# Performance work log

Measured on AMD Instinct MI355X. Metric: run time of the kernel, lower is better.

The kernel has to match this reference:

```python
import jax, jax.numpy as jnp
import numpy as np
import math

B_GRAPHS = 256
L_NODES = 64
N_NODES = B_GRAPHS * L_NODES
N_EDGES = N_NODES * 4
HEADS = 8
D_INNER = 512
N_DAGS = 1
DIAMETER = 64


def setup_inputs() -> dict:
    key = jax.random.key(0)
    ks = jax.random.split(key, 8)
    x = jax.random.normal(ks[0], (N_NODES, D_INNER), jnp.float32)
    B = jax.random.normal(ks[1], (N_NODES, D_INNER), jnp.float32)
    C = jax.random.normal(ks[2], (N_NODES, D_INNER), jnp.float32)
    dt = jax.random.normal(ks[3], (N_NODES, N_DAGS * HEADS * 2), jnp.float32)
    dt_edge = jax.random.normal(ks[4], (N_EDGES, N_DAGS * HEADS), jnp.float32)
    # DAG edges: within each graph, src_local < dst_local (gap 1..7) -> strictly upper triangular
    u = jax.random.randint(ks[5], (N_EDGES,), 0, L_NODES - 1)
    gap = jax.random.randint(ks[6], (N_EDGES,), 1, 8)
    v = jnp.minimum(u + gap, L_NODES - 1)
    graph = jnp.arange(N_EDGES) // (N_EDGES // B_GRAPHS)
    edge_index = jnp.stack([graph * L_NODES + u, graph * L_NODES + v]).astype(jnp.int32)
    data_batch = (jnp.arange(N_NODES) // L_NODES).astype(jnp.int32)
    dag_masks = jnp.ones((N_DAGS, N_EDGES), jnp.float32)
    # dt_bias init as in module __init__ (inverse softplus of dt in [1e-3, 1e-1])
    rng = np.random.default_rng(0)
    dtv = np.exp(rng.uniform(size=(HEADS,)) * (math.log(0.1) - math.log(0.001)) + math.log(0.001))
    dtv = np.clip(dtv, 1e-4, None)
    dt_bias = jnp.asarray(dtv + np.log(-np.expm1(-dtv)), jnp.float32)
    D = jnp.ones((HEADS,), jnp.float32)
    return dict(x=x, B=B, C=C, dt=dt, dt_edge=dt_edge, dt_bias=dt_bias, D=D,
                dag_masks=dag_masks, edge_index=edge_index, data_batch=data_batch,
                diameter=DIAMETER)


def _repeated_squaring_inverse(A, diam):
    # (I - A)^{-1} = prod_k (I + A^{2^k}) for nilpotent A; O(log diam) matmuls
    j = 2 ** int(math.ceil(math.log2(diam)))
    I = jnp.eye(A.shape[-1], dtype=A.dtype)
    last = A
    M = I + A
    for _ in range(2, int(math.log2(j)) + 1):
        last = last @ last
        M = M @ (I + last)
    return M


def reference(x, B, C, dt, dt_edge, dt_bias, D, dag_masks, edge_index, data_batch, diameter):
    N, din = x.shape
    g, E = dag_masks.shape
    n = dt_bias.shape[0]
    b = int(data_batch[-1]) + 1
    l = N // b  # equal-size graphs -> dense batching is a reshape, mask all-True
    h = din // n
    src, dst = edge_index[0], edge_index[1]

    # dt_node: (N, g*n*c) -> (c, g, n, N); softplus(dt + bias)
    c = dt.shape[1] // (g * n)
    dtn = dt.reshape(N, g, n, c).transpose(3, 1, 2, 0)
    dtn = jax.nn.softplus(dtn + dt_bias[None, None, :, None])
    dte = dt_edge.reshape(E, g, n).transpose(1, 2, 0)  # (g,n,E)
    dte = jax.nn.softplus(dte + dt_bias[None, :, None])

    dt_s, dt_t = dtn[0], dtn[1]
    dt_sum = (dt_s[:, :, src] + dt_t[:, :, dst] + dte) / np.sqrt(3.0)  # (g,n,E)
    dt_exp = jnp.exp(-dt_sum)
    msk = dag_masks[:, None, :]
    dt_sum = dt_sum * msk
    dt_exp = dt_exp * msk

    # dense adjacency with per-edge attrs; note 'b l1 l2 (g n) -> b g n l2 l1' transpose
    b_e = src // l
    sl = src % l
    dl = dst % l
    attr = dt_exp.transpose(2, 0, 1).reshape(E, g * n)
    adj = jnp.zeros((b, l, l, g * n), x.dtype).at[b_e, sl, dl].add(attr)
    A = adj.reshape(b, l, l, g, n).transpose(0, 3, 4, 2, 1)  # (b,g,n,l,l)

    # normalize_mat: sqrt outer product of in-degree counts, clamped at 1
    ec = jnp.zeros((g, N), x.dtype).at[:, dst].add(dag_masks)
    ec_dense = ec.T.reshape(b, l, g)
    outer = jnp.sqrt(jnp.einsum('blg,btg->bglt', ec_dense, ec_dense))
    outer = jnp.where(outer < 1.0, 1.0, outer)
    A = A / outer[:, :, None]

    dnorm = jnp.zeros((g, n, N), x.dtype).at[:, :, dst].add(dt_sum)
    dnorm = dnorm.transpose(2, 0, 1).reshape(b, l, g, n).transpose(0, 2, 3, 1)  # (b,g,n,l)

    A2 = A.reshape(b, g * n, l, l).astype(jnp.float32)
    L = _repeated_squaring_inverse(A2, int(diameter))
    L = L.reshape(b, g, n, l, l) * dnorm[..., None]

    x4 = x.reshape(b, l, n, h).transpose(0, 2, 1, 3)  # (b,n,l,h)
    B3 = B.reshape(b, l, -1)
    C3 = C.reshape(b, l, -1)
    # y = einsum(C,L,B,x) with B/C broadcast over (g,n): fold C.B^T into L
    CB = jnp.einsum('bld,btd->blt', C3, B3)
    M = L * CB[:, None, None]
    y = jnp.einsum('bgnlt,bnth->bgnlh', M, x4)
    y = y + x4[:, None] * D[None, None, :, None, None]
    y = y.transpose(0, 3, 1, 2, 4).reshape(N, g, n * h)  # b g n l h -> (N, g, n*h)
    y = y.sum(axis=1) / np.sqrt(g)
    return y
```

## Files before the change

kernel.cpp:

```cpp
#include <hip/hip_runtime.h>
#include <math.h>

#define NGRAPH 256
#define LNODE  64
#define HEADS  8
#define DIN    512
#define EPG    256
#define NEDGE  65536

typedef short bf16x8 __attribute__((ext_vector_type(8)));
typedef float f32x4 __attribute__((ext_vector_type(4)));

__device__ __forceinline__ float softplusf(float v) {
    return (v > 20.f) ? v : log1pf(expf(v));
}
__device__ __forceinline__ unsigned short f2bf(float f) {
    union { float f; unsigned u; } c; c.f = f;
    unsigned r = c.u + 0x7fffu + ((c.u >> 16) & 1u);
    return (unsigned short)(r >> 16);
}
__device__ __forceinline__ float bf2f(unsigned short h) {
    union { float f; unsigned u; } c; c.u = ((unsigned)h) << 16;
    return c.f;
}

__global__ __launch_bounds__(256) void cb_kernel(const float* __restrict__ Bm,
                                                 const float* __restrict__ Cm,
                                                 float* __restrict__ CBp,
                                                 int dper, int tposed) {
    int b = blockIdx.x;
    int slice = blockIdx.y;
    __shared__ float Cs[64 * 68];
    __shared__ float Bs[64 * 68];
    int tid = threadIdx.x;
    int ti = tid >> 4, tj = tid & 15;
    float acc[4][4] = {};
    const float* Cg = Cm + (size_t)b * 64 * DIN;
    const float* Bg = Bm + (size_t)b * 64 * DIN;
    int d_lo = slice * dper;
    for (int d0 = d_lo; d0 < d_lo + dper; d0 += 64) {
        __syncthreads();
        #pragma unroll
        for (int k = 0; k < 4; ++k) {
            int f = k * 256 + tid;
            int row = f >> 4;
            int c4 = (f & 15) << 2;
            *(float4*)(Cs + row * 68 + c4) = *(const float4*)(Cg + row * DIN + d0 + c4);
            *(float4*)(Bs + row * 68 + c4) = *(const float4*)(Bg + row * DIN + d0 + c4);
        }
        __syncthreads();
        for (int d = 0; d < 64; d += 4) {
            float4 cr[4], br[4];
            #pragma unroll
            for (int r = 0; r < 4; ++r) cr[r] = *(const float4*)(Cs + (4 * ti + r) * 68 + d);
            #pragma unroll
            for (int c = 0; c < 4; ++c) br[c] = *(const float4*)(Bs + (4 * tj + c) * 68 + d);
            #pragma unroll
            for (int r = 0; r < 4; ++r)
                #pragma unroll
                for (int c = 0; c < 4; ++c)
                    acc[r][c] += cr[r].x * br[c].x + cr[r].y * br[c].y +
                                 cr[r].z * br[c].z + cr[r].w * br[c].w;
        }
    }
    float* outp = CBp + ((size_t)slice * NGRAPH + b) * 4096;
    if (!tposed) {
        #pragma unroll
        for (int r = 0; r < 4; ++r)
            *(float4*)(outp + (4 * ti + r) * 64 + 4 * tj) =
                make_float4(acc[r][0], acc[r][1], acc[r][2], acc[r][3]);
    } else {
        #pragma unroll
        for (int r = 0; r < 4; ++r)
            #pragma unroll
            for (int c = 0; c < 4; ++c)
                outp[(4 * tj + c) * 64 + (4 * ti + r)] = acc[r][c];
    }
}

__global__ __launch_bounds__(256, 5) void fused2_kernel(const float* __restrict__ x,
                                                        const float* __restrict__ dt,
                                                        const float* __restrict__ dt_edge,
                                                        const float* __restrict__ dt_bias,
                                                        const float* __restrict__ Dp,
                                                        const float* __restrict__ dag_masks,
                                                        const int* __restrict__ edge_index,
                                                        const float* __restrict__ CBp,
                                                        float* __restrict__ out,
                                                        int nslice) {
    int b = blockIdx.x;
    int head = blockIdx.y;
    __shared__ unsigned short CBsh[64 * 64];
    __shared__ unsigned short Wl[64 * 72];
    __shared__ unsigned short Xt[64 * 66];
    __shared__ float Ab[512];
    __shared__ float dnsh[64];
    __shared__ float ecsh[64];
    __shared__ float dts[64];
    __shared__ float dtt[64];
    int tid = threadIdx.x;
    int w = tid >> 6;
    int lane = tid & 63;
    float bias = dt_bias[head];
    const float* xg0 = x + (size_t)b * 64 * DIN + head * 64;

    if (w == 0) {
        for (int it = 0; it < 16; ++it) {
            int s4 = it * 64 + lane;
            float4 v = *(const float4*)(CBp + (size_t)b * 4096 + s4 * 4);
            for (int s = 1; s < nslice; ++s) {
                float4 p = *(const float4*)(CBp + ((size_t)s * NGRAPH + b) * 4096 + s4 * 4);
                v.x += p.x; v.y += p.y; v.z += p.z; v.w += p.w;
            }
            unsigned short* q = &CBsh[s4 * 4];
            q[0] = f2bf(v.x); q[1] = f2bf(v.y); q[2] = f2bf(v.z); q[3] = f2bf(v.w);
        }
    } else {
        for (int t = w - 1; t < 64; t += 3) {
            float v = xg0[(size_t)t * DIN + lane];
            Xt[lane * 66 + t] = f2bf(v);
        }
        if (w == 1) {
            int node = b * 64 + lane;
            dts[lane] = softplusf(dt[node * 16 + head * 2 + 0] + bias);
            dtt[lane] = softplusf(dt[node * 16 + head * 2 + 1] + bias);
        } else if (w == 2) {
            #pragma unroll
            for (int k = 0; k < 8; ++k) Ab[k * 64 + lane] = 0.f;
        } else {
            dnsh[lane] = 0.f;
            ecsh[lane] = 0.f;
        }
    }
    __syncthreads();

    {
        int e = b * EPG + tid;
        int sl = edge_index[e] & 63;
        int dl = edge_index[NEDGE + e] & 63;
        float mk = dag_masks[e];
        float de = softplusf(dt_edge[e * HEADS + head] + bias);
        float dsum = (dts[sl] + dtt[dl] + de) * 0.57735026918962576451f;
        float dexp = expf(-dsum);
        atomicAdd(&Ab[dl * 8 + (dl - sl)], dexp * mk);
        atomicAdd(&dnsh[dl], dsum * mk);
        atomicAdd(&ecsh[dl], mk);
    }
    __syncthreads();

    for (int k = tid; k < 512; k += 256) {
        int i = k >> 3, d = k & 7;
        int src = i - d;
        if (d >= 1 && src >= 0) {
            float den = sqrtf(ecsh[i] * ecsh[src]);
            if (den < 1.f) den = 1.f;
            Ab[k] = Ab[k] / den;
        }
    }
    __syncthreads();

    int m = lane & 15;
    int quad = lane >> 4;
    union { bf16x8 v; unsigned u[4]; } bf[4][2];
    #pragma unroll
    for (int eb = 0; eb < 4; ++eb) {
        int n66 = (eb * 16 + m) * 66;
        #pragma unroll
        for (int h = 0; h < 2; ++h) {
            int base = n66 + h * 32 + quad * 8;
            #pragma unroll
            for (int c = 0; c < 4; ++c)
                bf[eb][h].u[c] = *(const unsigned*)(&Xt[base + 2 * c]);
        }
    }
    if (w == 0) {
        int j = lane;
        float Dh = Dp[head];
        float mwin[7] = {0.f, 0.f, 0.f, 0.f, 0.f, 0.f, 0.f};
        for (int i = 0; i < 64; ++i) {
            float mi = (j == i) ? 1.f : 0.f;
            #pragma unroll
            for (int s = 0; s < 7; ++s) mi += Ab[i * 8 + s + 1] * mwin[s];
            float wv = mi * bf2f(CBsh[i * 64 + j]) * dnsh[i];
            if (j == i) wv += Dh;
            Wl[i * 72 + j] = f2bf(wv);
            #pragma unroll
            for (int s = 6; s > 0; --s) mwin[s] = mwin[s - 1];
            mwin[0] = mi;
        }
    }
    __syncthreads();

    {
        bf16x8 a0 = *(const bf16x8*)(&Wl[(16 * w + m) * 72 + quad * 8]);
        bf16x8 a1 = *(const bf16x8*)(&Wl[(16 * w + m) * 72 + 32 + quad * 8]);
        float* og = out + ((size_t)b * 64) * DIN + head * 64;
        #pragma unroll
        for (int eb = 0; eb < 4; ++eb) {
            f32x4 acc = {0.f, 0.f, 0.f, 0.f};
            acc = __builtin_amdgcn_mfma_f32_16x16x32_bf16(a0, bf[eb][0].v, acc, 0, 0, 0);
            acc = __builtin_amdgcn_mfma_f32_16x16x32_bf16(a1, bf[eb][1].v, acc, 0, 0, 0);
            #pragma unroll
            for (int r = 0; r < 4; ++r) {
                int row = 16 * w + quad * 4 + r;
                og[(size_t)row * DIN + eb * 16 + m] = acc[r];
            }
        }
    }
}

__global__ __launch_bounds__(256, 4) void fused_kernel(const float* __restrict__ x,
                                                       const float* __restrict__ dt,
                                                       const float* __restrict__ dt_edge,
                                                       const float* __restrict__ dt_bias,
                                                       const float* __restrict__ Dp,
                                                       const float* __restrict__ dag_masks,
                                                       const int* __restrict__ edge_index,
                                                       const float* __restrict__ CBt,
                                                       float* __restrict__ out,
                                                       int nslice) {
    int b = blockIdx.x;
    int head = blockIdx.y;
    __shared__ float Ab[64 * 8];
    __shared__ float Mt[64 * 68];
    __shared__ float Xs[64 * 64];
    __shared__ float dnsh[64];
    __shared__ float ecsh[64];
    __shared__ float dts[64];
    __shared__ float dtt[64];
    int tid = threadIdx.x;

    int t4 = tid >> 2;
    int ib = (tid & 3) << 4;
    float4 cbsum[4];
    #pragma unroll
    for (int g = 0; g < 4; ++g) cbsum[g] = make_float4(0.f, 0.f, 0.f, 0.f);
    for (int s = 0; s < nslice; ++s) {
        const float* p = CBt + ((size_t)s * NGRAPH + b) * 4096 + t4 * 64 + ib;
        #pragma unroll
        for (int g = 0; g < 4; ++g) {
            float4 v = *(const float4*)(p + 4 * g);
            cbsum[g].x += v.x; cbsum[g].y += v.y; cbsum[g].z += v.z; cbsum[g].w += v.w;
        }
    }
    const float* xg0 = x + ((size_t)b * 64) * DIN + head * 64;
    #pragma unroll
    for (int k = 0; k < 4; ++k) {
        int s = k * 256 + tid;
        int row = s >> 4;
        int c4 = (s & 15) << 2;
        *(float4*)(Xs + row * 64 + c4) = *(const float4*)(xg0 + (size_t)row * DIN + c4);
    }
    for (int k = tid; k < 512; k += 256) Ab[k] = 0.f;
    float bias = dt_bias[head];
    if (tid < 64) {
        dnsh[tid] = 0.f;
        ecsh[tid] = 0.f;
        int node = b * 64 + tid;
        dts[tid] = softplusf(dt[node * 16 + head * 2 + 0] + bias);
        dtt[tid] = softplusf(dt[node * 16 + head * 2 + 1] + bias);
    }
    __syncthreads();
    {
        int e = b * EPG + tid;
        int sl = edge_index[e] & 63;
        int dl = edge_index[NEDGE + e] & 63;
        float mk = dag_masks[e];
        float de = softplusf(dt_edge[e * HEADS + head] + bias);
        float dsum = (dts[sl] + dtt[dl] + de) * 0.57735026918962576451f;
        float dexp = expf(-dsum);
        atomicAdd(&Ab[dl * 8 + (dl - sl)], dexp * mk);
        atomicAdd(&dnsh[dl], dsum * mk);
        atomicAdd(&ecsh[dl], mk);
    }
    __syncthreads();
    for (int k = tid; k < 512; k += 256) {
        int i = k >> 3, d = k & 7;
        int src = i - d;
        if (d >= 1 && src >= 0) {
            float den = sqrtf(ecsh[i] * ecsh[src]);
            if (den < 1.f) den = 1.f;
            Ab[k] = Ab[k] / den;
        }
    }
    __syncthreads();
    if (tid < 64) {
        int j = tid;
        float mwin[7] = {0.f, 0.f, 0.f, 0.f, 0.f, 0.f, 0.f};
        for (int i = 0; i < 64; ++i) {
            float mi = (j == i) ? 1.f : 0.f;
            #pragma unroll
            for (int s = 0; s < 7; ++s) mi += Ab[i * 8 + s + 1] * mwin[s];
            Mt[j * 65 + i] = mi;
            #pragma unroll
            for (int s = 6; s > 0; --s) mwin[s] = mwin[s - 1];
            mwin[0] = mi;
        }
    }
    __syncthreads();
    {
        float wv[16];
        #pragma unroll
        for (int g = 0; g < 4; ++g) {
            float4 dn4 = *(const float4*)(dnsh + ib + 4 * g);
            wv[4 * g + 0] = Mt[t4 * 65 + ib + 4 * g + 0] * cbsum[g].x * dn4.x;
            wv[4 * g + 1] = Mt[t4 * 65 + ib + 4 * g + 1] * cbsum[g].y * dn4.y;
            wv[4 * g + 2] = Mt[t4 * 65 + ib + 4 * g + 2] * cbsum[g].z * dn4.z;
            wv[4 * g + 3] = Mt[t4 * 65 + ib + 4 * g + 3] * cbsum[g].w * dn4.w;
        }
        __syncthreads();
        #pragma unroll
        for (int g = 0; g < 4; ++g)
            *(float4*)(Mt + t4 * 68 + ib + 4 * g) =
                make_float4(wv[4 * g + 0], wv[4 * g + 1], wv[4 * g + 2], wv[4 * g + 3]);
    }
    __syncthreads();
    int ti = tid >> 4, tj = tid & 15;
    float acc[4][4] = {};
    #pragma unroll 4
    for (int t = 0; t < 64; ++t) {
        float4 w4 = *(const float4*)(Mt + t * 68 + 4 * ti);
        float4 xv = *(const float4*)(Xs + t * 64 + 4 * tj);
        acc[0][0] += w4.x * xv.x; acc[0][1] += w4.x * xv.y; acc[0][2] += w4.x * xv.z; acc[0][3] += w4.x * xv.w;
        acc[1][0] += w4.y * xv.x; acc[1][1] += w4.y * xv.y; acc[1][2] += w4.y * xv.z; acc[1][3] += w4.y * xv.w;
        acc[2][0] += w4.z * xv.x; acc[2][1] += w4.z * xv.y; acc[2][2] += w4.z * xv.z; acc[2][3] += w4.z * xv.w;
        acc[3][0] += w4.w * xv.x; acc[3][1] += w4.w * xv.y; acc[3][2] += w4.w * xv.z; acc[3][3] += w4.w * xv.w;
    }
    float Dh = Dp[head];
    #pragma unroll
    for (int r = 0; r < 4; ++r) {
        int i = 4 * ti + r;
        float4 xres = *(const float4*)(Xs + i * 64 + 4 * tj);
        float4 v;
        v.x = acc[r][0] + xres.x * Dh;
        v.y = acc[r][1] + xres.y * Dh;
        v.z = acc[r][2] + xres.z * Dh;
        v.w = acc[r][3] + xres.w * Dh;
        *(float4*)(out + ((size_t)(b * 64 + i)) * DIN + head * 64 + 4 * tj) = v;
    }
}

extern "C" void kernel_launch(void* const* d_in, const int* in_sizes, int n_in,
                              void* d_out, int out_size, void* d_ws, size_t ws_size,
                              hipStream_t stream) {
    const float* x        = (const float*)d_in[0];
    const float* Bm       = (const float*)d_in[1];
    const float* Cm       = (const float*)d_in[2];
    const float* dt       = (const float*)d_in[3];
    const float* dt_edge  = (const float*)d_in[4];
    const float* dt_bias  = (const float*)d_in[5];
    const float* Dp       = (const float*)d_in[6];
    const float* dag_mask = (const float*)d_in[7];
    const int*   edge_idx = (const int*)d_in[8];
    float* out = (float*)d_out;

    const size_t CBSLICE = (size_t)NGRAPH * 4096 * 4;
    float* CBp = (float*)d_ws;

    if (ws_size >= 2 * CBSLICE) {
        int nslice = 2;
        cb_kernel<<<dim3(NGRAPH, nslice), 256, 0, stream>>>(Bm, Cm, CBp, DIN / nslice, 0);
        fused2_kernel<<<dim3(NGRAPH, HEADS), 256, 0, stream>>>(x, dt, dt_edge, dt_bias, Dp,
                                                               dag_mask, edge_idx, CBp, out, nslice);
    } else {
        int nslice = 1;
        cb_kernel<<<dim3(NGRAPH, nslice), 256, 0, stream>>>(Bm, Cm, CBp, DIN / nslice, 1);
        fused_kernel<<<dim3(NGRAPH, HEADS), 256, 0, stream>>>(x, dt, dt_edge, dt_bias, Dp,
                                                              dag_mask, edge_idx, CBp, out, nslice);
    }
}
```

Baseline: 198.7 us.

## Stream CB rows into registers during recurrence, drop CB shared buffer

Wave 0 no longer stages the reduced CB tile into shared memory up front. It now prefetches CB rows from global memory in double-buffered register chunks of 16 while it runs the triangular recurrence. The x-tile transpose load is spread evenly over all four waves, and the occupancy hint is raised from 5 to 6 blocks, which the smaller shared-memory footprint makes possible. The CB sum now assumes at most two slices, so it silently gives wrong results if nslice > 2, and register pressure in wave 0 goes up.

```diff
diff --git a/kernel.cpp b/kernel.cpp
--- a/kernel.cpp
+++ b/kernel.cpp
@@ -78,7 +78,7 @@
     }
 }
 
-__global__ __launch_bounds__(256, 5) void fused2_kernel(const float* __restrict__ x,
+__global__ __launch_bounds__(256, 6) void fused2_kernel(const float* __restrict__ x,
                                                         const float* __restrict__ dt,
                                                         const float* __restrict__ dt_edge,
                                                         const float* __restrict__ dt_bias,
@@ -90,7 +90,6 @@
                                                         int nslice) {
     int b = blockIdx.x;
     int head = blockIdx.y;
-    __shared__ unsigned short CBsh[64 * 64];
     __shared__ unsigned short Wl[64 * 72];
     __shared__ unsigned short Xt[64 * 66];
     __shared__ float Ab[512];
@@ -104,33 +103,19 @@
     float bias = dt_bias[head];
     const float* xg0 = x + (size_t)b * 64 * DIN + head * 64;
 
-    if (w == 0) {
-        for (int it = 0; it < 16; ++it) {
-            int s4 = it * 64 + lane;
-            float4 v = *(const float4*)(CBp + (size_t)b * 4096 + s4 * 4);
-            for (int s = 1; s < nslice; ++s) {
-                float4 p = *(const float4*)(CBp + ((size_t)s * NGRAPH + b) * 4096 + s4 * 4);
-                v.x += p.x; v.y += p.y; v.z += p.z; v.w += p.w;
-            }
-            unsigned short* q = &CBsh[s4 * 4];
-            q[0] = f2bf(v.x); q[1] = f2bf(v.y); q[2] = f2bf(v.z); q[3] = f2bf(v.w);
-        }
-    } else {
-        for (int t = w - 1; t < 64; t += 3) {
-            float v = xg0[(size_t)t * DIN + lane];
-            Xt[lane * 66 + t] = f2bf(v);
-        }
-        if (w == 1) {
-            int node = b * 64 + lane;
-            dts[lane] = softplusf(dt[node * 16 + head * 2 + 0] + bias);
-            dtt[lane] = softplusf(dt[node * 16 + head * 2 + 1] + bias);
-        } else if (w == 2) {
-            #pragma unroll
-            for (int k = 0; k < 8; ++k) Ab[k * 64 + lane] = 0.f;
-        } else {
-            dnsh[lane] = 0.f;
-            ecsh[lane] = 0.f;
-        }
+    #pragma unroll
+    for (int it = 0; it < 16; ++it) {
+        int t = it * 4 + w;
+        Xt[lane * 66 + t] = f2bf(xg0[(size_t)t * DIN + lane]);
+    }
+    for (int k = tid; k < 512; k += 256) Ab[k] = 0.f;
+    if (tid < 64) {
+        int node = b * 64 + tid;
+        dts[tid] = softplusf(dt[node * 16 + head * 2 + 0] + bias);
+        dtt[tid] = softplusf(dt[node * 16 + head * 2 + 1] + bias);
+    } else if (tid < 128) {
+        dnsh[tid - 64] = 0.f;
+        ecsh[tid - 64] = 0.f;
     }
     __syncthreads();
 
@@ -162,31 +147,62 @@
     int m = lane & 15;
     int quad = lane >> 4;
     union { bf16x8 v; unsigned u[4]; } bf[4][2];
-    #pragma unroll
-    for (int eb = 0; eb < 4; ++eb) {
-        int n66 = (eb * 16 + m) * 66;
-        #pragma unroll
-        for (int h = 0; h < 2; ++h) {
-            int base = n66 + h * 32 + quad * 8;
-            #pragma unroll
-            for (int c = 0; c < 4; ++c)
-                bf[eb][h].u[c] = *(const unsigned*)(&Xt[base + 2 * c]);
-        }
-    }
-    if (w == 0) {
+    if (w != 0) {
+        #pragma unroll
+        for (int eb = 0; eb < 4; ++eb) {
+            int n66 = (eb * 16 + m) * 66;
+            #pragma unroll
+            for (int h = 0; h < 2; ++h) {
+                int base = n66 + h * 32 + quad * 8;
+                #pragma unroll
+                for (int c = 0; c < 4; ++c)
+                    bf[eb][h].u[c] = *(const unsigned*)(&Xt[base + 2 * c]);
+            }
+        }
+    } else {
         int j = lane;
         float Dh = Dp[head];
+        const float* cbA = CBp + (size_t)b * 4096 + j;
+        const float* cbB = cbA + (size_t)NGRAPH * 4096;
+        bool two = (nslice > 1);
+        float buf[2][16];
+        #pragma unroll
+        for (int u = 0; u < 16; ++u)
+            buf[0][u] = cbA[u * 64] + (two ? cbB[u * 64] : 0.f);
         float mwin[7] = {0.f, 0.f, 0.f, 0.f, 0.f, 0.f, 0.f};
-        for (int i = 0; i < 64; ++i) {
-            float mi = (j == i) ? 1.f : 0.f;
-            #pragma unroll
-            for (int s = 0; s < 7; ++s) mi += Ab[i * 8 + s + 1] * mwin[s];
-            float wv = mi * bf2f(CBsh[i * 64 + j]) * dnsh[i];
-            if (j == i) wv += Dh;
-            Wl[i * 72 + j] = f2bf(wv);
-            #pragma unroll
-            for (int s = 6; s > 0; --s) mwin[s] = mwin[s - 1];
-            mwin[0] = mi;
+        #pragma unroll
+        for (int g = 0; g < 4; ++g) {
+            if (g < 3) {
+                #pragma unroll
+                for (int u = 0; u < 16; ++u) {
+                    int i = (g + 1) * 16 + u;
+                    buf[(g + 1) & 1][u] = cbA[i * 64] + (two ? cbB[i * 64] : 0.f);
+                }
+            }
+            #pragma unroll
+            for (int u = 0; u < 16; ++u) {
+                int i = g * 16 + u;
+                float mi = (j == i) ? 1.f : 0.f;
+                #pragma unroll
+                for (int s = 0; s < 7; ++s) mi += Ab[i * 8 + s + 1] * mwin[s];
+                float wv = mi * buf[g & 1][u] * dnsh[i];
+                if (j == i) wv += Dh;
+                Wl[i * 72 + j] = f2bf(wv);
+                #pragma unroll
+                for (int s = 6; s > 0; --s) mwin[s] = mwin[s - 1];
+                mwin[0] = mi;
+            }
+        }
+        #pragma unroll
+        for (int eb = 0; eb < 4; ++eb) {
+            int n66 = (eb * 16 + m) * 66;
+            #pragma unroll
+            for (int h = 0; h < 2; ++h) {
+                int base = n66 + h * 32 + quad * 8;
+                #pragma unroll
+                for (int c = 0; c < 4; ++c)
+                    bf[eb][h].u[c] = *(const unsigned*)(&Xt[base + 2 * c]);
+            }
         }
     }
     __syncthreads();
```

Result: no change. 200.6 us (+1.0%).
